# Kernel optimization log

Hardware: AMD Instinct MI355X
Metric: run time of the kernel (lower is better)

## Reference

```python
import jax, jax.numpy as jnp
import numpy as np

N_GRID = 4096    # SOS grid is N_GRID x N_GRID; len(x_vec)=len(y_vec)=N_GRID
N_POINTS = 2048  # number of ray angles (thetas)
N_INT = 4096     # integration samples per ray


def setup_inputs() -> dict:
    key = jax.random.key(0)
    k1, = jax.random.split(key, 1)
    # speed-of-sound map ~ 1400..1600 m/s (tissue-like)
    SOS = 1400.0 + 200.0 * jax.random.uniform(k1, (N_GRID, N_GRID), dtype=jnp.float32)
    x_vec = jnp.linspace(-0.06, 0.06, N_GRID, dtype=jnp.float32)
    y_vec = jnp.linspace(-0.06, 0.06, N_GRID, dtype=jnp.float32)
    thetas = jnp.linspace(0.0, 2.0 * np.pi, N_POINTS, dtype=jnp.float32)
    x = jnp.float32(0.012)   # source point inside the body (r < R_body)
    y = jnp.float32(-0.008)
    R_body = jnp.float32(0.04)
    v0 = jnp.float32(1500.0)
    return dict(x=x, y=y, SOS=SOS, x_vec=x_vec, y_vec=y_vec,
                thetas=thetas, R_body=R_body, v0=v0)


def reference(x, y, SOS, x_vec, y_vec, thetas, R_body, v0):
    th = thetas[:, None]                                  # [P,1]
    r = jnp.sqrt(x ** 2 + y ** 2)
    phi = jnp.arctan2(x, y)
    s = r * jnp.sin(th - phi)                             # [P,1]
    c = r * jnp.cos(th - phi)                             # cos is even: == cos(phi-th)
    disc = R_body ** 2 - s ** 2
    # branch 1: point inside the body (disc >= 0 guaranteed; clamp for safety)
    l_in = jnp.sqrt(jnp.maximum(disc, 0.0)) + c
    # branch 2: point outside the body, mask rays that intersect the circle
    mask = (jnp.cos(phi - th) >= 0) & (R_body >= jnp.abs(s))
    l_out = jnp.sqrt(jnp.maximum(disc * mask, 0.0)) + c * mask
    l = jnp.where(r < R_body, l_in, l_out)                # [P,1] chord length per ray

    steps = jnp.linspace(0.0, 1.0, N_INT, dtype=SOS.dtype)[None, :]  # [1,N]
    dx = x_vec[1] - x_vec[0]
    dy = y_vec[1] - y_vec[0]
    xs = x - l * steps * jnp.sin(th)                      # [P,N] ray sample x-coords
    ys = y - l * steps * jnp.cos(th)                      # [P,N] ray sample y-coords
    j_index = jnp.clip(jnp.round((xs - x_vec[0]) / dx).astype(jnp.int32), 0, SOS.shape[1] - 1)
    i_index = jnp.clip(jnp.round(-(ys - y_vec[-1]) / dy).astype(jnp.int32), 0, SOS.shape[0] - 1)

    f = 1.0 - v0 / SOS[i_index, j_index]                  # [P,N] irregular 2D gather
    xcoord = l * steps                                    # [P,N] non-uniform abscissa
    seg = xcoord[:, 1:] - xcoord[:, :-1]
    wf = jnp.sum(0.5 * (f[:, 1:] + f[:, :-1]) * seg, axis=1)  # trapezoid along dim=1
    return thetas, wf
```

## Files before the change

kernel.cpp:

```cpp
#include <hip/hip_runtime.h>
#include <math.h>

#define NT 256

__global__ __launch_bounds__(NT) void wf_kernel(
    const float* __restrict__ xp, const float* __restrict__ yp,
    const float* __restrict__ SOS, const float* __restrict__ x_vec,
    const float* __restrict__ y_vec, const float* __restrict__ thetas,
    const float* __restrict__ Rp, const float* __restrict__ v0p,
    float* __restrict__ out, int n_grid, int n_theta, int n_int)
{
    const int t   = blockIdx.x;
    const int tid = threadIdx.x;
    if (t >= n_theta) return;

    const float x  = xp[0];
    const float y  = yp[0];
    const float R  = Rp[0];
    const float v0 = v0p[0];
    const float th = thetas[t];

    const float x0    = x_vec[0];
    const float dxg   = x_vec[1] - x_vec[0];
    const float ylast = y_vec[n_grid - 1];
    const float dyg   = y_vec[1] - y_vec[0];

    const float r   = sqrtf(x * x + y * y);
    const float phi = atan2f(x, y);
    float sdp, cdp;
    sincosf(th - phi, &sdp, &cdp);
    const float s    = r * sdp;
    const float c    = r * cdp;
    const float disc = R * R - s * s;
    const float l_in = sqrtf(fmaxf(disc, 0.0f)) + c;
    const bool  mask  = (cdp >= 0.0f) && (R >= fabsf(s));
    const float l_out = mask ? l_in : 0.0f;
    const float l     = (r < R) ? l_in : l_out;

    float sth, cth;
    sincosf(th, &sth, &cth);

    const float inv = 1.0f / (float)(n_int - 1);

    float acc = 0.0f;
    for (int k = tid; k < n_int; k += NT) {
        float step = (float)k * inv;
        float ls   = l * step;
        float xs   = x - ls * sth;
        float ys   = y - ls * cth;
        int j = (int)rintf((xs - x0) / dxg);
        int i = (int)rintf(-(ys - ylast) / dyg);
        j = min(max(j, 0), n_grid - 1);
        i = min(max(i, 0), n_grid - 1);
        float f = 1.0f - v0 / SOS[(size_t)i * (size_t)n_grid + (size_t)j];
        float w = (k == 0 || k == n_int - 1) ? 0.5f : 1.0f;
        acc += w * f;
    }

    #pragma unroll
    for (int off = 32; off > 0; off >>= 1)
        acc += __shfl_down(acc, off, 64);

    __shared__ float wsum[NT / 64];
    const int wave = tid >> 6;
    const int lane = tid & 63;
    if (lane == 0) wsum[wave] = acc;
    __syncthreads();

    if (tid == 0) {
        float total = 0.0f;
        #pragma unroll
        for (int w = 0; w < NT / 64; ++w) total += wsum[w];
        out[n_theta + t] = total * l * inv;
        out[t]           = th;
    }
}

extern "C" void kernel_launch(void* const* d_in, const int* in_sizes, int n_in,
                              void* d_out, int out_size, void* d_ws, size_t ws_size,
                              hipStream_t stream) {
    const float* xp     = (const float*)d_in[0];
    const float* yp     = (const float*)d_in[1];
    const float* SOS    = (const float*)d_in[2];
    const float* x_vec  = (const float*)d_in[3];
    const float* y_vec  = (const float*)d_in[4];
    const float* thetas = (const float*)d_in[5];
    const float* Rp     = (const float*)d_in[6];
    const float* v0p    = (const float*)d_in[7];
    float* out = (float*)d_out;

    const int n_grid  = in_sizes[3];
    const int n_theta = in_sizes[5];
    const int n_int   = 4096;

    wf_kernel<<<n_theta, NT, 0, stream>>>(xp, yp, SOS, x_vec, y_vec, thetas,
                                          Rp, v0p, out, n_grid, n_theta, n_int);
}
```

Measured before the change: 119.1 us.

## Remap blocks across XCDs, strength-reduce index math, fully unroll gather loop

Block IDs are permuted so that consecutive ray angles, whose rays touch nearby SOS cells, land on the same XCD under round-robin dispatch, which should improve L2 locality of the gathers. Per-sample index computation is reduced to one FMA per coordinate using precomputed affine coefficients. The loop is fully unrolled with a compile-time sample count so more gathers can be in flight, and the division is replaced with a hardware reciprocal. The reciprocal trades a little accuracy, and FMA-based index rounding may occasionally pick a different cell than the reference at rounding boundaries.

```diff
diff --git a/kernel.cpp b/kernel.cpp
--- a/kernel.cpp
+++ b/kernel.cpp
@@ -2,15 +2,24 @@
 #include <math.h>
 
 #define NT 256
+#define N_INT_C 4096
+#define ITERS (N_INT_C / NT)
 
 __global__ __launch_bounds__(NT) void wf_kernel(
     const float* __restrict__ xp, const float* __restrict__ yp,
     const float* __restrict__ SOS, const float* __restrict__ x_vec,
     const float* __restrict__ y_vec, const float* __restrict__ thetas,
     const float* __restrict__ Rp, const float* __restrict__ v0p,
-    float* __restrict__ out, int n_grid, int n_theta, int n_int)
+    float* __restrict__ out, int n_grid, int n_theta)
 {
-    const int t   = blockIdx.x;
+    int bid = blockIdx.x;
+    int t;
+    if ((n_theta & 7) == 0) {
+        int chunk = n_theta >> 3;
+        t = (bid & 7) * chunk + (bid >> 3);
+    } else {
+        t = bid;
+    }
     const int tid = threadIdx.x;
     if (t >= n_theta) return;
 
@@ -40,20 +49,28 @@
     float sth, cth;
     sincosf(th, &sth, &cth);
 
-    const float inv = 1.0f / (float)(n_int - 1);
+    const float inv   = 1.0f / (float)(N_INT_C - 1);
+    const float lstep = l * inv;
+
+    const float A = (x - x0) / dxg;
+    const float P = lstep * sth / dxg;
+    const float C = (ylast - y) / dyg;
+    const float Q = lstep * cth / dyg;
+
+    const int gmax = n_grid - 1;
 
     float acc = 0.0f;
-    for (int k = tid; k < n_int; k += NT) {
-        float step = (float)k * inv;
-        float ls   = l * step;
-        float xs   = x - ls * sth;
-        float ys   = y - ls * cth;
-        int j = (int)rintf((xs - x0) / dxg);
-        int i = (int)rintf(-(ys - ylast) / dyg);
-        j = min(max(j, 0), n_grid - 1);
-        i = min(max(i, 0), n_grid - 1);
-        float f = 1.0f - v0 / SOS[(size_t)i * (size_t)n_grid + (size_t)j];
-        float w = (k == 0 || k == n_int - 1) ? 0.5f : 1.0f;
+    #pragma unroll
+    for (int u = 0; u < ITERS; ++u) {
+        const int k = u * NT + tid;
+        const float fk = (float)k;
+        int j = (int)rintf(fmaf(-P, fk, A));
+        int i = (int)rintf(fmaf( Q, fk, C));
+        j = min(max(j, 0), gmax);
+        i = min(max(i, 0), gmax);
+        float sos = SOS[i * n_grid + j];
+        float f = fmaf(-v0, __builtin_amdgcn_rcpf(sos), 1.0f);
+        float w = (k == 0 || k == N_INT_C - 1) ? 0.5f : 1.0f;
         acc += w * f;
     }
 
@@ -71,7 +88,7 @@
         float total = 0.0f;
         #pragma unroll
         for (int w = 0; w < NT / 64; ++w) total += wsum[w];
-        out[n_theta + t] = total * l * inv;
+        out[n_theta + t] = total * lstep;
         out[t]           = th;
     }
 }
@@ -91,8 +108,7 @@
 
     const int n_grid  = in_sizes[3];
     const int n_theta = in_sizes[5];
-    const int n_int   = 4096;
 
     wf_kernel<<<n_theta, NT, 0, stream>>>(xp, yp, SOS, x_vec, y_vec, thetas,
-                                          Rp, v0p, out, n_grid, n_theta, n_int);
+                                          Rp, v0p, out, n_grid, n_theta);
 }
```

Result: no change. 117.8 us (-1.1%).
